# Performance work log

Measured on AMD Instinct MI355X. Metric: run time of the kernel, lower is better.

Reference implementation:

```python
import jax, jax.numpy as jnp
import numpy as np

EMBED_DIM = 1024
HIDDEN_DIM = 4096
NUM_EXPERTS = 8
TOP_K = 2


def setup_inputs() -> dict:
    key = jax.random.key(0)
    ks = jax.random.split(key, 5)
    x = jax.random.normal(ks[0], (2, 2048, EMBED_DIM), dtype=jnp.float32)
    Wg = jax.random.normal(ks[1], (EMBED_DIM, NUM_EXPERTS), dtype=jnp.float32) * 0.02
    W1 = jax.random.normal(ks[2], (NUM_EXPERTS, EMBED_DIM, HIDDEN_DIM), dtype=jnp.float32) * 0.02
    W3 = jax.random.normal(ks[3], (NUM_EXPERTS, EMBED_DIM, HIDDEN_DIM), dtype=jnp.float32) * 0.02
    W2 = jax.random.normal(ks[4], (NUM_EXPERTS, HIDDEN_DIM, EMBED_DIM), dtype=jnp.float32) * 0.02
    return {"x": x, "Wg": Wg, "W1": W1, "W3": W3, "W2": W2}


def reference(x, Wg, W1, W3, W2):
    # Gate: linear projection to num_experts logits
    gate = jnp.einsum("bsd,de->bse", x, Wg)  # [B,S,E]
    top_vals, top_idx = jax.lax.top_k(gate, TOP_K)  # [B,S,K]
    sel_w = jax.nn.softmax(top_vals, axis=-1)  # softmax over top-k values
    # Scatter selected weights into dense [B,S,E] (zeros for unselected experts)
    dense_w = jnp.sum(
        jax.nn.one_hot(top_idx, NUM_EXPERTS, dtype=sel_w.dtype) * sel_w[..., None],
        axis=-2,
    )  # [B,S,E]
    # Per-expert SwiGLU FFN; weight=0 for tokens not routed to expert e,
    # so the weighted-sum form is mathematically identical to masked dispatch.
    out = jnp.zeros_like(x)
    for e in range(NUM_EXPERTS):
        h = jax.nn.swish(jnp.einsum("bsd,dh->bsh", x, W1[e])) * jnp.einsum(
            "bsd,dh->bsh", x, W3[e]
        )
        out = out + dense_w[..., e:e + 1] * jnp.einsum("bsh,hd->bsd", h, W2[e])
    return out
```

## Files before the change

kernel.cpp:

```cpp
#include <hip/hip_runtime.h>
#include <hip/hip_bf16.h>
#include <stdint.h>

#define D_EMBED 1024
#define D_HID   4096
#define N_TOK   4096
#define N_EXP   8
#define CAP     4096
#define NROWA   8448

typedef __attribute__((ext_vector_type(4))) float f32x4;
typedef __attribute__((ext_vector_type(8))) short bf16x8;

__device__ __forceinline__ unsigned short f2bf(float f) {
    unsigned int u = __builtin_bit_cast(unsigned int, f);
    u += 0x7fffu + ((u >> 16) & 1u);
    return (unsigned short)(u >> 16);
}

__device__ __forceinline__ void gload_lds16(const void* g, void* l) {
    __builtin_amdgcn_global_load_lds(
        (const __attribute__((address_space(1))) unsigned int*)g,
        (__attribute__((address_space(3))) unsigned int*)l,
        16, 0, 0);
}

__global__ __launch_bounds__(256) void pack_w(const float* __restrict__ W,
                                              unsigned short* __restrict__ out, int R, int C) {
    int e = blockIdx.z, kb = blockIdx.y, cb = blockIdx.x;
    const float* Wp = W + (size_t)e * R * C + (size_t)(kb * 64) * C + cb * 64;
    unsigned short* op = out + (size_t)e * R * C;
    __shared__ unsigned short lds[64][72];
    int t = threadIdx.x;
    int r = t >> 2;
    int c0 = (t & 3) << 4;
    const float* src = Wp + (size_t)r * C + c0;
#pragma unroll
    for (int i = 0; i < 2; ++i) {
        f32x4 a = *reinterpret_cast<const f32x4*>(src + i * 8);
        f32x4 b = *reinterpret_cast<const f32x4*>(src + i * 8 + 4);
        bf16x8 o;
        o[0]=(short)f2bf(a[0]); o[1]=(short)f2bf(a[1]); o[2]=(short)f2bf(a[2]); o[3]=(short)f2bf(a[3]);
        o[4]=(short)f2bf(b[0]); o[5]=(short)f2bf(b[1]); o[6]=(short)f2bf(b[2]); o[7]=(short)f2bf(b[3]);
        *reinterpret_cast<bf16x8*>(&lds[r][c0 + i * 8]) = o;
    }
    __syncthreads();
#pragma unroll
    for (int i = 0; i < 2; ++i) {
        int cell = i * 256 + t;
        int ksl = cell >> 6, col = cell & 63;
        bf16x8 o;
#pragma unroll
        for (int j = 0; j < 8; ++j) o[j] = (short)lds[ksl * 8 + j][col];
        *reinterpret_cast<bf16x8*>(op + ((size_t)(kb * 8 + ksl) * C + cb * 64 + col) * 8) = o;
    }
}

__global__ __launch_bounds__(256) void pack_w13(const float* __restrict__ W1,
                                                const float* __restrict__ W3,
                                                unsigned short* __restrict__ out) {
    int e = blockIdx.z, kb = blockIdx.y, cb = blockIdx.x;
    size_t ebase = (size_t)e * D_EMBED * D_HID;
    const float* b1 = W1 + ebase + (size_t)(kb * 64) * D_HID + cb * 32;
    const float* b3 = W3 + ebase + (size_t)(kb * 64) * D_HID + cb * 32;
    unsigned short* op = out + (size_t)e * D_EMBED * 2 * D_HID;
    __shared__ unsigned short lds[64][72];
    int t = threadIdx.x;
    int r = t >> 2, ck = t & 3;
    const float* src = (ck >= 2 ? b3 : b1) + (size_t)r * D_HID + (ck & 1) * 16;
#pragma unroll
    for (int i = 0; i < 2; ++i) {
        f32x4 a = *reinterpret_cast<const f32x4*>(src + i * 8);
        f32x4 b = *reinterpret_cast<const f32x4*>(src + i * 8 + 4);
        bf16x8 o;
        o[0]=(short)f2bf(a[0]); o[1]=(short)f2bf(a[1]); o[2]=(short)f2bf(a[2]); o[3]=(short)f2bf(a[3]);
        o[4]=(short)f2bf(b[0]); o[5]=(short)f2bf(b[1]); o[6]=(short)f2bf(b[2]); o[7]=(short)f2bf(b[3]);
        *reinterpret_cast<bf16x8*>(&lds[r][ck * 16 + i * 8]) = o;
    }
    __syncthreads();
#pragma unroll
    for (int i = 0; i < 2; ++i) {
        int cell = i * 256 + t;
        int ksl = cell >> 6, pcp = cell & 63;
        int lcol = ((pcp >> 4) & 1) * 32 + ((pcp >> 5) & 1) * 16 + (pcp & 15);
        bf16x8 o;
#pragma unroll
        for (int j = 0; j < 8; ++j) o[j] = (short)lds[ksl * 8 + j][lcol];
        *reinterpret_cast<bf16x8*>(op + ((size_t)(kb * 8 + ksl) * (2 * D_HID) + cb * 64 + pcp) * 8) = o;
    }
}

__global__ __launch_bounds__(256) void gate_kernel(const float* __restrict__ x,
                                                   const float* __restrict__ Wg,
                                                   int* __restrict__ counts,
                                                   int* __restrict__ toks,
                                                   float* __restrict__ wgts,
                                                   int* __restrict__ slots) {
    int wave = threadIdx.x >> 6;
    int lane = threadIdx.x & 63;
    int tok = blockIdx.x * 4 + wave;
    const float* xp = x + (size_t)tok * D_EMBED;
    float acc[8] = {0, 0, 0, 0, 0, 0, 0, 0};
#pragma unroll
    for (int i = 0; i < 16; ++i) {
        int d = lane + 64 * i;
        float xv = xp[d];
        f32x4 w0 = *reinterpret_cast<const f32x4*>(Wg + (size_t)d * 8);
        f32x4 w1 = *reinterpret_cast<const f32x4*>(Wg + (size_t)d * 8 + 4);
        acc[0] += xv * w0[0]; acc[1] += xv * w0[1]; acc[2] += xv * w0[2]; acc[3] += xv * w0[3];
        acc[4] += xv * w1[0]; acc[5] += xv * w1[1]; acc[6] += xv * w1[2]; acc[7] += xv * w1[3];
    }
#pragma unroll
    for (int e = 0; e < 8; ++e)
        for (int s = 32; s; s >>= 1) acc[e] += __shfl_xor(acc[e], s, 64);
    if (lane == 0) {
        int i0 = 0; float v0 = acc[0];
#pragma unroll
        for (int e = 1; e < 8; ++e) if (acc[e] > v0) { v0 = acc[e]; i0 = e; }
        int i1 = -1; float v1 = -1e30f;
#pragma unroll
        for (int e = 0; e < 8; ++e) if (e != i0 && acc[e] > v1) { v1 = acc[e]; i1 = e; }
        float ex = __expf(v1 - v0);
        float w0 = 1.0f / (1.0f + ex);
        float w1 = 1.0f - w0;
        int p0 = atomicAdd(&counts[i0], 1);
        toks[i0 * CAP + p0] = tok; wgts[i0 * CAP + p0] = w0; slots[i0 * CAP + p0] = 0;
        int p1 = atomicAdd(&counts[i1], 1);
        toks[i1 * CAP + p1] = tok; wgts[i1 * CAP + p1] = w1; slots[i1 * CAP + p1] = 1;
    }
}

__global__ void prefix_kernel(const int* __restrict__ counts, int* __restrict__ offsets) {
    if (threadIdx.x == 0) {
        int s = 0;
        for (int e = 0; e < N_EXP; ++e) { offsets[e] = s; s += counts[e]; }
    }
}

__global__ __launch_bounds__(256) void build_map_kernel(const int* __restrict__ counts,
                                                        const int* __restrict__ offsets,
                                                        const int* __restrict__ toks,
                                                        const int* __restrict__ slots,
                                                        int* __restrict__ tok2row) {
    int i = blockIdx.x * 256 + threadIdx.x;
    int e = i >> 12, pos = i & (CAP - 1);
    if (pos < counts[e])
        tok2row[toks[i] * 2 + slots[i]] = offsets[e] + pos;
}

__global__ __launch_bounds__(256) void gather_x_kernel(
    const float* __restrict__ x,
    const int* __restrict__ counts, const int* __restrict__ offsets,
    const int* __restrict__ toks,
    unsigned short* __restrict__ xg) {
    int rt = blockIdx.x;
    int e = -1, base = 0, rowbase = 0, cnt = 0;
    for (int ee = 0; ee < N_EXP; ++ee) {
        int c = counts[ee];
        int nt = (c + 63) >> 6;
        if (rt < base + nt) { e = ee; rowbase = (rt - base) << 6; cnt = c; break; }
        base += nt;
    }
    if (e < 0) return;
    int off = offsets[e];
    int kb = blockIdx.y;
    __shared__ unsigned short lds[64][72];
    int t = threadIdx.x;
    int r = t >> 2, ck = t & 3;
    int pos = rowbase + r;
    unsigned short tmp[16];
    if (pos < cnt) {
        int tok = toks[e * CAP + pos];
        const float* src = x + (size_t)tok * D_EMBED + kb * 64 + ck * 16;
#pragma unroll
        for (int i = 0; i < 4; ++i) {
            f32x4 v = *reinterpret_cast<const f32x4*>(src + i * 4);
#pragma unroll
            for (int j = 0; j < 4; ++j) tmp[i * 4 + j] = f2bf(v[j]);
        }
    } else {
#pragma unroll
        for (int i = 0; i < 16; ++i) tmp[i] = 0;
    }
#pragma unroll
    for (int i = 0; i < 16; ++i) lds[r][ck * 16 + i] = tmp[i];
    __syncthreads();
    int sl = t >> 5, rr = (t & 31) * 2;
#pragma unroll
    for (int w = 0; w < 2; ++w) {
        int rw = rr + w;
        if (rowbase + rw >= cnt) continue;
        bf16x8 o;
#pragma unroll
        for (int j = 0; j < 8; ++j) o[j] = (short)lds[rw][sl * 8 + j];
        *reinterpret_cast<bf16x8*>(xg + ((size_t)(kb * 8 + sl) * NROWA + off + rowbase + rw) * 8) = o;
    }
}

__global__ __launch_bounds__(512, 1) void gemm1_kernel(
    const unsigned short* __restrict__ xg,
    const unsigned short* __restrict__ wt13,
    const int* __restrict__ counts, const int* __restrict__ offsets,
    const float* __restrict__ wgts,
    unsigned short* __restrict__ hp) {
    int rt = blockIdx.y;
    int e = -1, base = 0, rowbase = 0, cnt = 0;
#pragma unroll 1
    for (int ee = 0; ee < N_EXP; ++ee) {
        int c = counts[ee];
        int nt = (c + 255) >> 8;
        if (rt < base + nt) { e = ee; rowbase = (rt - base) << 8; cnt = c; break; }
        base += nt;
    }
    if (e < 0) return;
    int off = offsets[e];
    int colp = blockIdx.x * 256;

    __shared__ __align__(16) char lds[4][32768];

    int t = threadIdx.x, lane = t & 63, w = t >> 6;
    int wr = w >> 2, wc = w & 3;
    int q = lane >> 4, p = lane & 15;
    int w2 = w * 2;

    const unsigned short* wB = wt13 + (size_t)e * D_EMBED * 2 * D_HID;
    const unsigned short* pA = xg + (size_t)(off + rowbase) * 8;

    f32x4 acc[8][4] = {};

    auto SC = [&](int h, int c) {
        char* Ls = &lds[h & 3][0];
        size_t gs = (size_t)(h * 4 + (c >> 2));
        gload_lds16(pA + (gs * NROWA + (c & 3) * 64 + lane) * 8, Ls + c * 1024);
        gload_lds16(wB + (gs * (2 * D_HID) + colp + (c & 3) * 64 + lane) * 8,
                    Ls + 16384 + c * 1024);
    };

    SC(0, w2); SC(0, w2 + 1);
    SC(1, w2); SC(1, w2 + 1);
#pragma unroll 1
    for (int h = 0; h < 32; ++h) {
        if (h < 30) asm volatile("s_waitcnt vmcnt(4)" ::: "memory");
        else        asm volatile("s_waitcnt vmcnt(0)" ::: "memory");
        __builtin_amdgcn_s_barrier();
        asm volatile("" ::: "memory");
        const char* L = &lds[h & 3][0];
        if (h < 30) SC(h + 2, w2);
        bf16x8 af0[4], bfr[4];
#pragma unroll
        for (int m = 0; m < 4; ++m)
            af0[m] = *reinterpret_cast<const bf16x8*>(L + q * 4096 + (wr * 128 + m * 16 + p) * 16);
#pragma unroll
        for (int n = 0; n < 4; ++n)
            bfr[n] = *reinterpret_cast<const bf16x8*>(L + 16384 + q * 4096 + (wc * 64 + n * 16 + p) * 16);
        __builtin_amdgcn_s_setprio(1);
#pragma unroll
        for (int n = 0; n < 4; ++n)
#pragma unroll
            for (int m = 0; m < 4; ++m)
                acc[m][n] = __builtin_amdgcn_mfma_f32_16x16x32_bf16(af0[m], bfr[n], acc[m][n], 0, 0, 0);
        __builtin_amdgcn_s_setprio(0);
        if (h < 30) SC(h + 2, w2 + 1);
        bf16x8 af1[4];
#pragma unroll
        for (int m = 0; m < 4; ++m)
            af1[m] = *reinterpret_cast<const bf16x8*>(L + q * 4096 + (wr * 128 + (m + 4) * 16 + p) * 16);
        __builtin_amdgcn_s_setprio(1);
#pragma unroll
        for (int n = 0; n < 4; ++n)
#pragma unroll
            for (int m = 0; m < 4; ++m)
                acc[m + 4][n] = __builtin_amdgcn_mfma_f32_16x16x32_bf16(af1[m], bfr[n], acc[m + 4][n], 0, 0, 0);
        __builtin_amdgcn_s_setprio(0);
        asm volatile("" ::: "memory");
    }

#pragma unroll
    for (int m = 0; m < 8; ++m) {
#pragma unroll
        for (int reg = 0; reg < 4; ++reg) {
            int rl = wr * 128 + m * 16 + q * 4 + reg;
            int grow = rowbase + rl;
            if (grow >= cnt) continue;
            float wgt = wgts[e * CAP + grow];
            size_t row = (size_t)(off + grow);
#pragma unroll
            for (int np = 0; np < 2; ++np) {
                float a1 = acc[m][2 * np][reg];
                float a3 = acc[m][2 * np + 1][reg];
                float hv = (a1 / (1.0f + __expf(-a1))) * a3 * wgt;
                int rc = (blockIdx.x * 8 + wc * 2 + np) * 16 + p;
                hp[((size_t)(rc >> 3) * NROWA + row) * 8 + (rc & 7)] = f2bf(hv);
            }
        }
    }
}

__global__ __launch_bounds__(512, 1) void gemm2_kernel(
    const unsigned short* __restrict__ hp,
    const unsigned short* __restrict__ wt2,
    const int* __restrict__ counts, const int* __restrict__ offsets,
    float* __restrict__ pbuf) {
    int rt = blockIdx.y;
    int e = -1, base = 0, rowbase = 0, cnt = 0;
#pragma unroll 1
    for (int ee = 0; ee < N_EXP; ++ee) {
        int c = counts[ee];
        int nt = (c + 255) >> 8;
        if (rt < base + nt) { e = ee; rowbase = (rt - base) << 8; cnt = c; break; }
        base += nt;
    }
    if (e < 0) return;
    int off = offsets[e];
    int colb = blockIdx.x * 256;
    int s2 = blockIdx.z;

    __shared__ __align__(16) char lds[4][32768];

    int t = threadIdx.x, lane = t & 63, w = t >> 6;
    int wr = w >> 2, wc = w & 3;
    int q = lane >> 4, p = lane & 15;
    int w2 = w * 2;

    const unsigned short* wB = wt2 + (size_t)e * D_HID * D_EMBED;
    const unsigned short* pA = hp + (size_t)(off + rowbase) * 8;

    f32x4 acc[8][4] = {};

    auto SC = [&](int h, int c) {
        char* Ls = &lds[h & 3][0];
        size_t gs = (size_t)(s2 * 128 + h * 4 + (c >> 2));
        gload_lds16(pA + (gs * NROWA + (c & 3) * 64 + lane) * 8, Ls + c * 1024);
        gload_lds16(wB + (gs * D_EMBED + colb + (c & 3) * 64 + lane) * 8,
                    Ls + 16384 + c * 1024);
    };

    SC(0, w2); SC(0, w2 + 1);
    SC(1, w2); SC(1, w2 + 1);
#pragma unroll 1
    for (int h = 0; h < 32; ++h) {
        if (h < 30) asm volatile("s_waitcnt vmcnt(4)" ::: "memory");
        else        asm volatile("s_waitcnt vmcnt(0)" ::: "memory");
        __builtin_amdgcn_s_barrier();
        asm volatile("" ::: "memory");
        const char* L = &lds[h & 3][0];
        if (h < 30) SC(h + 2, w2);
        bf16x8 af0[4], bfr[4];
#pragma unroll
        for (int m = 0; m < 4; ++m)
            af0[m] = *reinterpret_cast<const bf16x8*>(L + q * 4096 + (wr * 128 + m * 16 + p) * 16);
#pragma unroll
        for (int n = 0; n < 4; ++n)
            bfr[n] = *reinterpret_cast<const bf16x8*>(L + 16384 + q * 4096 + (wc * 64 + n * 16 + p) * 16);
        __builtin_amdgcn_s_setprio(1);
#pragma unroll
        for (int n = 0; n < 4; ++n)
#pragma unroll
            for (int m = 0; m < 4; ++m)
                acc[m][n] = __builtin_amdgcn_mfma_f32_16x16x32_bf16(af0[m], bfr[n], acc[m][n], 0, 0, 0);
        __builtin_amdgcn_s_setprio(0);
        if (h < 30) SC(h + 2, w2 + 1);
        bf16x8 af1[4];
#pragma unroll
        for (int m = 0; m < 4; ++m)
            af1[m] = *reinterpret_cast<const bf16x8*>(L + q * 4096 + (wr * 128 + (m + 4) * 16 + p) * 16);
        __builtin_amdgcn_s_setprio(1);
#pragma unroll
        for (int n = 0; n < 4; ++n)
#pragma unroll
            for (int m = 0; m < 4; ++m)
                acc[m + 4][n] = __builtin_amdgcn_mfma_f32_16x16x32_bf16(af1[m], bfr[n], acc[m + 4][n], 0, 0, 0);
        __builtin_amdgcn_s_setprio(0);
        asm volatile("" ::: "memory");
    }

    float* pb = pbuf + (size_t)s2 * 8192 * D_EMBED;
#pragma unroll
    for (int m = 0; m < 8; ++m)
#pragma unroll
        for (int reg = 0; reg < 4; ++reg) {
            int rl = wr * 128 + m * 16 + q * 4 + reg;
            int grow = rowbase + rl;
            if (grow >= cnt) continue;
            float* dst = pb + (size_t)(off + grow) * D_EMBED + colb + wc * 64;
#pragma unroll
            for (int n = 0; n < 4; ++n) dst[n * 16 + p] = acc[m][n][reg];
        }
}

__global__ __launch_bounds__(256) void combine_kernel(const float* __restrict__ pbuf,
                                                      const int* __restrict__ tok2row,
                                                      float* __restrict__ out) {
    int i = blockIdx.x * 256 + threadIdx.x;
    int tok = i >> 8, c = (i & 255) * 4;
    int r0 = tok2row[tok * 2], r1 = tok2row[tok * 2 + 1];
    const size_t SP = (size_t)8192 * D_EMBED;
    f32x4 s = {0.f, 0.f, 0.f, 0.f};
#pragma unroll
    for (int sp = 0; sp < 4; ++sp) {
        f32x4 a = *reinterpret_cast<const f32x4*>(pbuf + sp * SP + (size_t)r0 * D_EMBED + c);
        f32x4 b = *reinterpret_cast<const f32x4*>(pbuf + sp * SP + (size_t)r1 * D_EMBED + c);
        s = s + a + b;
    }
    *reinterpret_cast<f32x4*>(out + (size_t)tok * D_EMBED + c) = s;
}

extern "C" void kernel_launch(void* const* d_in, const int* in_sizes, int n_in,
                              void* d_out, int out_size, void* d_ws, size_t ws_size,
                              hipStream_t stream) {
    const float* x  = (const float*)d_in[0];
    const float* Wg = (const float*)d_in[1];
    const float* W1 = (const float*)d_in[2];
    const float* W3 = (const float*)d_in[3];
    const float* W2 = (const float*)d_in[4];
    float* out = (float*)d_out;

    char* ws = (char*)d_ws;
    size_t szW = (size_t)N_EXP * D_EMBED * D_HID;
    unsigned short* wt13 = (unsigned short*)ws; ws += szW * 2 * 2;
    unsigned short* wt2  = (unsigned short*)ws; ws += szW * 2;
    unsigned short* hp   = (unsigned short*)ws; ws += (size_t)(D_HID / 8) * NROWA * 8 * 2;
    unsigned short* xg   = (unsigned short*)ws; ws += (size_t)(D_EMBED / 8) * NROWA * 8 * 2;
    int*   toks    = (int*)ws;   ws += (size_t)N_EXP * CAP * 4;
    float* wgts    = (float*)ws; ws += (size_t)N_EXP * CAP * 4;
    int*   slots   = (int*)ws;   ws += (size_t)N_EXP * CAP * 4;
    int*   tok2row = (int*)ws;   ws += (size_t)N_TOK * 2 * 4;
    int*   counts  = (int*)ws;   ws += 8 * 4;
    int*   offsets = (int*)ws;   ws += 8 * 4;
    float* pbuf = (float*)wt13;

    hipMemsetAsync(counts, 0, 8 * sizeof(int), stream);

    pack_w13<<<dim3(128, 16, N_EXP), 256, 0, stream>>>(W1, W3, wt13);
    pack_w<<<dim3(D_EMBED / 64, D_HID / 64, N_EXP), 256, 0, stream>>>(W2, wt2, D_HID, D_EMBED);
    gate_kernel<<<N_TOK / 4, 256, 0, stream>>>(x, Wg, counts, toks, wgts, slots);
    prefix_kernel<<<1, 64, 0, stream>>>(counts, offsets);
    build_map_kernel<<<(N_EXP * CAP) / 256, 256, 0, stream>>>(counts, offsets, toks, slots, tok2row);
    gather_x_kernel<<<dim3(136, D_EMBED / 64), 256, 0, stream>>>(x, counts, offsets, toks, xg);
    gemm1_kernel<<<dim3(32, 39), 512, 0, stream>>>(xg, wt13, counts, offsets, wgts, hp);
    gemm2_kernel<<<dim3(4, 39, 4), 512, 0, stream>>>(hp, wt2, counts, offsets, pbuf);
    combine_kernel<<<(N_TOK * 256) / 256, 256, 0, stream>>>(pbuf, tok2row, out);
}
```

Before: 550.3 us.

## Restructure GEMM main loops with early fragment loads and split-barrier staging

Both expert GEMM kernels now load all A and B fragments for a K-step from LDS before any MFMA, and split the MFMA work into two halves. A barrier sits after the fragment reads and another after the second staging issue. Staging switches from per-wave chunks to a flat per-thread layout, with a prologue wait and barrier ahead of the loop. The aim is to separate LDS reads from MFMA issue and overlap global-to-LDS loads with compute, at the cost of more fragment registers and an extra barrier per iteration.

```diff
diff --git a/kernel.cpp b/kernel.cpp
--- a/kernel.cpp
+++ b/kernel.cpp
@@ -221,56 +221,58 @@
     int t = threadIdx.x, lane = t & 63, w = t >> 6;
     int wr = w >> 2, wc = w & 3;
     int q = lane >> 4, p = lane & 15;
-    int w2 = w * 2;
 
     const unsigned short* wB = wt13 + (size_t)e * D_EMBED * 2 * D_HID;
     const unsigned short* pA = xg + (size_t)(off + rowbase) * 8;
 
     f32x4 acc[8][4] = {};
 
-    auto SC = [&](int h, int c) {
-        char* Ls = &lds[h & 3][0];
-        size_t gs = (size_t)(h * 4 + (c >> 2));
-        gload_lds16(pA + (gs * NROWA + (c & 3) * 64 + lane) * 8, Ls + c * 1024);
-        gload_lds16(wB + (gs * (2 * D_HID) + colp + (c & 3) * 64 + lane) * 8,
-                    Ls + 16384 + c * 1024);
+    auto STG = [&](int h, int j) {
+        char* L = &lds[h & 3][0];
+        int flat = j * 512 + t;
+        size_t gs = (size_t)(h * 4 + (flat >> 8));
+        int rc = flat & 255;
+        gload_lds16(pA + (gs * NROWA + rc) * 8, L + flat * 16);
+        gload_lds16(wB + (gs * (2 * D_HID) + colp + rc) * 8, L + 16384 + flat * 16);
     };
 
-    SC(0, w2); SC(0, w2 + 1);
-    SC(1, w2); SC(1, w2 + 1);
+    STG(0, 0); STG(0, 1); STG(1, 0); STG(1, 1);
+    asm volatile("s_waitcnt vmcnt(4)" ::: "memory");
+    __builtin_amdgcn_s_barrier();
+    asm volatile("" ::: "memory");
+
 #pragma unroll 1
     for (int h = 0; h < 32; ++h) {
-        if (h < 30) asm volatile("s_waitcnt vmcnt(4)" ::: "memory");
+        const char* L = &lds[h & 3][0];
+        if (h < 30) STG(h + 2, 0);
+        bf16x8 af[8], bf[4];
+#pragma unroll
+        for (int m = 0; m < 8; ++m)
+            af[m] = *reinterpret_cast<const bf16x8*>(L + (q * 256 + wr * 128 + m * 16 + p) * 16);
+#pragma unroll
+        for (int n = 0; n < 4; ++n)
+            bf[n] = *reinterpret_cast<const bf16x8*>(L + 16384 + (q * 256 + wc * 64 + n * 16 + p) * 16);
+        asm volatile("" ::: "memory");
+        __builtin_amdgcn_s_barrier();
+        __builtin_amdgcn_s_setprio(1);
+#pragma unroll
+        for (int n = 0; n < 2; ++n)
+#pragma unroll
+            for (int m = 0; m < 8; ++m)
+                acc[m][n] = __builtin_amdgcn_mfma_f32_16x16x32_bf16(af[m], bf[n], acc[m][n], 0, 0, 0);
+        __builtin_amdgcn_s_setprio(0);
+        asm volatile("" ::: "memory");
+        if (h < 30) asm volatile("s_waitcnt vmcnt(2)" ::: "memory");
         else        asm volatile("s_waitcnt vmcnt(0)" ::: "memory");
+        if (h < 30) STG(h + 2, 1);
+        asm volatile("" ::: "memory");
         __builtin_amdgcn_s_barrier();
-        asm volatile("" ::: "memory");
-        const char* L = &lds[h & 3][0];
-        if (h < 30) SC(h + 2, w2);
-        bf16x8 af0[4], bfr[4];
-#pragma unroll
-        for (int m = 0; m < 4; ++m)
-            af0[m] = *reinterpret_cast<const bf16x8*>(L + q * 4096 + (wr * 128 + m * 16 + p) * 16);
-#pragma unroll
-        for (int n = 0; n < 4; ++n)
-            bfr[n] = *reinterpret_cast<const bf16x8*>(L + 16384 + q * 4096 + (wc * 64 + n * 16 + p) * 16);
         __builtin_amdgcn_s_setprio(1);
 #pragma unroll
-        for (int n = 0; n < 4; ++n)
-#pragma unroll
-            for (int m = 0; m < 4; ++m)
-                acc[m][n] = __builtin_amdgcn_mfma_f32_16x16x32_bf16(af0[m], bfr[n], acc[m][n], 0, 0, 0);
-        __builtin_amdgcn_s_setprio(0);
-        if (h < 30) SC(h + 2, w2 + 1);
-        bf16x8 af1[4];
-#pragma unroll
-        for (int m = 0; m < 4; ++m)
-            af1[m] = *reinterpret_cast<const bf16x8*>(L + q * 4096 + (wr * 128 + (m + 4) * 16 + p) * 16);
-        __builtin_amdgcn_s_setprio(1);
-#pragma unroll
-        for (int n = 0; n < 4; ++n)
-#pragma unroll
-            for (int m = 0; m < 4; ++m)
-                acc[m + 4][n] = __builtin_amdgcn_mfma_f32_16x16x32_bf16(af1[m], bfr[n], acc[m + 4][n], 0, 0, 0);
+        for (int n = 2; n < 4; ++n)
+#pragma unroll
+            for (int m = 0; m < 8; ++m)
+                acc[m][n] = __builtin_amdgcn_mfma_f32_16x16x32_bf16(af[m], bf[n], acc[m][n], 0, 0, 0);
         __builtin_amdgcn_s_setprio(0);
         asm volatile("" ::: "memory");
     }
@@ -320,56 +322,58 @@
     int t = threadIdx.x, lane = t & 63, w = t >> 6;
     int wr = w >> 2, wc = w & 3;
     int q = lane >> 4, p = lane & 15;
-    int w2 = w * 2;
 
     const unsigned short* wB = wt2 + (size_t)e * D_HID * D_EMBED;
     const unsigned short* pA = hp + (size_t)(off + rowbase) * 8;
 
     f32x4 acc[8][4] = {};
 
-    auto SC = [&](int h, int c) {
-        char* Ls = &lds[h & 3][0];
-        size_t gs = (size_t)(s2 * 128 + h * 4 + (c >> 2));
-        gload_lds16(pA + (gs * NROWA + (c & 3) * 64 + lane) * 8, Ls + c * 1024);
-        gload_lds16(wB + (gs * D_EMBED + colb + (c & 3) * 64 + lane) * 8,
-                    Ls + 16384 + c * 1024);
+    auto STG = [&](int h, int j) {
+        char* L = &lds[h & 3][0];
+        int flat = j * 512 + t;
+        size_t gs = (size_t)(s2 * 128 + h * 4 + (flat >> 8));
+        int rc = flat & 255;
+        gload_lds16(pA + (gs * NROWA + rc) * 8, L + flat * 16);
+        gload_lds16(wB + (gs * D_EMBED + colb + rc) * 8, L + 16384 + flat * 16);
     };
 
-    SC(0, w2); SC(0, w2 + 1);
-    SC(1, w2); SC(1, w2 + 1);
+    STG(0, 0); STG(0, 1); STG(1, 0); STG(1, 1);
+    asm volatile("s_waitcnt vmcnt(4)" ::: "memory");
+    __builtin_amdgcn_s_barrier();
+    asm volatile("" ::: "memory");
+
 #pragma unroll 1
     for (int h = 0; h < 32; ++h) {
-        if (h < 30) asm volatile("s_waitcnt vmcnt(4)" ::: "memory");
+        const char* L = &lds[h & 3][0];
+        if (h < 30) STG(h + 2, 0);
+        bf16x8 af[8], bf[4];
+#pragma unroll
+        for (int m = 0; m < 8; ++m)
+            af[m] = *reinterpret_cast<const bf16x8*>(L + (q * 256 + wr * 128 + m * 16 + p) * 16);
+#pragma unroll
+        for (int n = 0; n < 4; ++n)
+            bf[n] = *reinterpret_cast<const bf16x8*>(L + 16384 + (q * 256 + wc * 64 + n * 16 + p) * 16);
+        asm volatile("" ::: "memory");
+        __builtin_amdgcn_s_barrier();
+        __builtin_amdgcn_s_setprio(1);
+#pragma unroll
+        for (int n = 0; n < 2; ++n)
+#pragma unroll
+            for (int m = 0; m < 8; ++m)
+                acc[m][n] = __builtin_amdgcn_mfma_f32_16x16x32_bf16(af[m], bf[n], acc[m][n], 0, 0, 0);
+        __builtin_amdgcn_s_setprio(0);
+        asm volatile("" ::: "memory");
+        if (h < 30) asm volatile("s_waitcnt vmcnt(2)" ::: "memory");
         else        asm volatile("s_waitcnt vmcnt(0)" ::: "memory");
+        if (h < 30) STG(h + 2, 1);
+        asm volatile("" ::: "memory");
         __builtin_amdgcn_s_barrier();
-        asm volatile("" ::: "memory");
-        const char* L = &lds[h & 3][0];
-        if (h < 30) SC(h + 2, w2);
-        bf16x8 af0[4], bfr[4];
-#pragma unroll
-        for (int m = 0; m < 4; ++m)
-            af0[m] = *reinterpret_cast<const bf16x8*>(L + q * 4096 + (wr * 128 + m * 16 + p) * 16);
-#pragma unroll
-        for (int n = 0; n < 4; ++n)
-            bfr[n] = *reinterpret_cast<const bf16x8*>(L + 16384 + q * 4096 + (wc * 64 + n * 16 + p) * 16);
         __builtin_amdgcn_s_setprio(1);
 #pragma unroll
-        for (int n = 0; n < 4; ++n)
-#pragma unroll
-            for (int m = 0; m < 4; ++m)
-                acc[m][n] = __builtin_amdgcn_mfma_f32_16x16x32_bf16(af0[m], bfr[n], acc[m][n], 0, 0, 0);
-        __builtin_amdgcn_s_setprio(0);
-        if (h < 30) SC(h + 2, w2 + 1);
-        bf16x8 af1[4];
-#pragma unroll
-        for (int m = 0; m < 4; ++m)
-            af1[m] = *reinterpret_cast<const bf16x8*>(L + q * 4096 + (wr * 128 + (m + 4) * 16 + p) * 16);
-        __builtin_amdgcn_s_setprio(1);
-#pragma unroll
-        for (int n = 0; n < 4; ++n)
-#pragma unroll
-            for (int m = 0; m < 4; ++m)
-                acc[m + 4][n] = __builtin_amdgcn_mfma_f32_16x16x32_bf16(af1[m], bfr[n], acc[m + 4][n], 0, 0, 0);
+        for (int n = 2; n < 4; ++n)
+#pragma unroll
+            for (int m = 0; m < 8; ++m)
+                acc[m][n] = __builtin_amdgcn_mfma_f32_16x16x32_bf16(af[m], bf[n], acc[m][n], 0, 0, 0);
         __builtin_amdgcn_s_setprio(0);
         asm volatile("" ::: "memory");
     }
```

Measured after the change: 542.4 us. Within noise of the previous version (-1.4%).
